# Performance work log

Hardware: AMD Instinct MI355X
Metric: run time of the kernel (lower is better)

Reference implementation:

```python
import jax, jax.numpy as jnp
import numpy as np

N_NODES = 100_000
N_EDGES = 1_600_000
D_IN = 128
D_HID = 64   # hard-coded hidden width in Embedder.__init__
D_OUT = 128  # embed_dim
N_GRAPHS = 512


def setup_inputs() -> dict:
    key = jax.random.key(0)
    ks = jax.random.split(key, 10)
    x = jax.random.normal(ks[0], (N_NODES, D_IN), dtype=jnp.float32)
    edge_index = jax.random.randint(ks[1], (2, N_EDGES), 0, N_NODES, dtype=jnp.int64)
    batch_index = jnp.sort(jax.random.randint(ks[2], (N_NODES,), 0, N_GRAPHS, dtype=jnp.int64))
    def glorot(k, fan_in, fan_out):
        s = 1.0 / np.sqrt(fan_in)
        return jax.random.uniform(k, (fan_in, fan_out), jnp.float32, -s, s)
    # layer 1: SAGEConv(D_IN -> D_HID); layer 2: SAGEConv(D_HID -> D_OUT)
    return {
        "x": x,
        "W1_l": glorot(ks[3], D_IN, D_HID),   # applied to mean-aggregated neighbors
        "W1_r": glorot(ks[4], D_IN, D_HID),   # applied to root node
        "b1": jnp.zeros((D_HID,), jnp.float32),
        "W2_l": glorot(ks[5], D_HID, D_OUT),
        "W2_r": glorot(ks[6], D_HID, D_OUT),
        "b2": jnp.zeros((D_OUT,), jnp.float32),
        "edge_index": edge_index,
        "batch_index": batch_index,
    }


def _sage_conv(x, edge_index, W_l, W_r, b):
    # PyG SAGEConv with mean aggregation:
    # out_i = (mean_{j in N(i)} x_j) @ W_l + x_i @ W_r + b
    src, dst = edge_index[0], edge_index[1]
    n = x.shape[0]
    agg = jax.ops.segment_sum(x[src], dst, num_segments=n)          # [N, F]
    deg = jax.ops.segment_sum(jnp.ones((src.shape[0],), x.dtype), dst, num_segments=n)
    mean_nbr = agg / jnp.maximum(deg, 1.0)[:, None]
    return mean_nbr @ W_l + x @ W_r + b


def reference(x, W1_l, W1_r, b1, W2_l, W2_r, b2, edge_index, batch_index):
    h = _sage_conv(x, edge_index, W1_l, W1_r, b1)
    h = jax.nn.relu(h)
    h = _sage_conv(h, edge_index, W2_l, W2_r, b2)
    # F.dropout(p=0.5, training=False) -> identity in eval mode
    # gap: global mean pool per graph
    sums = jax.ops.segment_sum(h, batch_index, num_segments=N_GRAPHS)
    cnts = jax.ops.segment_sum(jnp.ones((h.shape[0],), h.dtype), batch_index, num_segments=N_GRAPHS)
    return sums / jnp.maximum(cnts, 1.0)[:, None]
```

## Files before the change

kernel.cpp:

```cpp
#include <hip/hip_runtime.h>

#define NN   100000
#define NE   1600000
#define DIN  128
#define DH   64
#define DOUT 128
#define NG   512

#define NB   391
#define EPB  6250
#define MSZ  (NB*256)

typedef short short8 __attribute__((ext_vector_type(8)));
typedef float floatx4 __attribute__((ext_vector_type(4)));

__device__ __forceinline__ unsigned short f2bf(float f) {
  unsigned b = __float_as_uint(f);
  b += 0x7FFF + ((b >> 16) & 1);
  return (unsigned short)(b >> 16);
}
__device__ __forceinline__ float bflo(unsigned u) {
  return __uint_as_float(u << 16);
}
__device__ __forceinline__ float bfhi(unsigned u) {
  return __uint_as_float(u & 0xFFFF0000u);
}
__device__ __forceinline__ unsigned pack2(float a, float b) {
  return (unsigned)f2bf(a) | ((unsigned)f2bf(b) << 16);
}

__global__ __launch_bounds__(256) void prep_kernel(
    const int* __restrict__ dst, int* __restrict__ cnt,
    const float* __restrict__ W1l, const float* __restrict__ W1r,
    short* __restrict__ wfrag, const int* __restrict__ batch,
    int* __restrict__ gs) {
  __shared__ int h[NB];
  int b = blockIdx.x;
  if (b < 256) {
    for (int i = threadIdx.x; i < NB; i += 256) h[i] = 0;
    __syncthreads();
    int start = b * EPB, end = start + EPB;
    for (int e = start + threadIdx.x; e < end; e += 256)
      atomicAdd(&h[dst[e] >> 8], 1);
    __syncthreads();
    for (int bb = threadIdx.x; bb < NB; bb += 256)
      cnt[bb * 256 + b] = h[bb];
  } else if (b == 256) {
    for (int i = threadIdx.x; i < DIN * DH; i += 256) {
      int k = i >> 6, n = i & 63;
      int kt = k >> 5, kin = k & 31;
      int lane = ((kin >> 3) << 4) | (n & 15);
      int j8 = kin & 7;
      int jt = n >> 4;
      float wl = W1l[i], wr = W1r[i];
      unsigned bl_ = __float_as_uint(wl);
      unsigned br_ = __float_as_uint(wr);
      short hl = (short)(bl_ >> 16);
      short hr = (short)(br_ >> 16);
      float rl = wl - __uint_as_float(bl_ & 0xFFFF0000u);
      float rr = wr - __uint_as_float(br_ & 0xFFFF0000u);
      short ll = (short)(__float_as_uint(rl) >> 16);
      short lr = (short)(__float_as_uint(rr) >> 16);
      int base0 = (((kt * 2 + 0) * 4 + jt) * 2) * 512 + lane * 8 + j8;
      int base1 = (((kt * 2 + 1) * 4 + jt) * 2) * 512 + lane * 8 + j8;
      wfrag[base0]       = hl;
      wfrag[base0 + 512] = ll;
      wfrag[base1]       = hr;
      wfrag[base1 + 512] = lr;
    }
  } else {
    for (int g = threadIdx.x; g <= NG; g += 256) {
      if (g == NG) { gs[NG] = NN; continue; }
      int lo = 0, hi = NN;
      while (lo < hi) {
        int mid = (lo + hi) >> 1;
        if (batch[mid] < g) lo = mid + 1; else hi = mid;
      }
      gs[g] = lo;
    }
  }
}

__global__ __launch_bounds__(256) void reduce_kernel(
    const int* __restrict__ cnt, int* __restrict__ partials) {
  __shared__ int s[256];
  int i = blockIdx.x * 256 + threadIdx.x;
  s[threadIdx.x] = cnt[i];
  __syncthreads();
  for (int off = 128; off > 0; off >>= 1) {
    if (threadIdx.x < off) s[threadIdx.x] += s[threadIdx.x + off];
    __syncthreads();
  }
  if (threadIdx.x == 0) partials[blockIdx.x] = s[0];
}

__global__ __launch_bounds__(256) void scanpart_kernel(int* __restrict__ partials) {
  __shared__ int s[NB];
  for (int i = threadIdx.x; i < NB; i += 256) s[i] = partials[i];
  __syncthreads();
  if (threadIdx.x == 0) {
    int run = 0;
    for (int i = 0; i < NB; ++i) { int v = s[i]; s[i] = run; run += v; }
  }
  __syncthreads();
  for (int i = threadIdx.x; i < NB; i += 256) partials[i] = s[i];
}

__global__ __launch_bounds__(256) void scanfinal_kernel(
    const int* __restrict__ cnt, const int* __restrict__ partials,
    int* __restrict__ scanned) {
  __shared__ int s[256];
  int t = threadIdx.x;
  int i = blockIdx.x * 256 + t;
  int c = cnt[i];
  s[t] = c;
  __syncthreads();
  for (int off = 1; off < 256; off <<= 1) {
    int v = (t >= off) ? s[t - off] : 0;
    __syncthreads();
    s[t] += v;
    __syncthreads();
  }
  scanned[i] = s[t] - c + partials[blockIdx.x];
}

__global__ __launch_bounds__(256, 4) void proj_part_kernel(
    const int* __restrict__ src, const int* __restrict__ dst,
    const int* __restrict__ scanned, int* __restrict__ part,
    const float* __restrict__ x, const short* __restrict__ wfrag,
    const float* __restrict__ b1, unsigned short* __restrict__ xlb,
    unsigned short* __restrict__ xrb) {
  __shared__ short sB[16384];
  if (blockIdx.x < 256) {
    int* cur = (int*)sB;
    for (int i = threadIdx.x; i < NB; i += 256)
      cur[i] = scanned[i * 256 + blockIdx.x];
    __syncthreads();
    int start = blockIdx.x * EPB, end = start + EPB;
    for (int e = start + threadIdx.x; e < end; e += 256) {
      int d = dst[e], s = src[e];
      int pos = atomicAdd(&cur[d >> 8], 1);
      part[pos] = ((d & 255) << 17) | s;
    }
    return;
  }
  int wave = threadIdx.x >> 6;
  int lane = threadIdx.x & 63;
  int m = lane & 15, q = lane >> 4;
  int tpair = (blockIdx.x - 256) * 4 + wave;
  int tile0 = tpair * 2, tile1 = tile0 + 1;
  bool act0 = tile0 < 6250;
  bool act1 = tile1 < 6250;
  int t0c = act0 ? tile0 : 6249;
  int t1c = act1 ? tile1 : 6249;

  int r0 = t0c * 16 + m;
  int r1 = t1c * 16 + m;
  const float4* xa = (const float4*)x + (size_t)r0 * 32 + q * 2;
  const float4* xb = (const float4*)x + (size_t)r1 * 32 + q * 2;

  floatx4 acc0[8], acc1[8];
#pragma unroll
  for (int a = 0; a < 8; ++a) {
    acc0[a] = (floatx4){0.f, 0.f, 0.f, 0.f};
    acc1[a] = (floatx4){0.f, 0.f, 0.f, 0.f};
  }

  const float4* wf4 = (const float4*)wfrag;
  float4* sB4 = (float4*)sB;

#pragma unroll 1
  for (int stage = 0; stage < 2; ++stage) {
    if (stage) __syncthreads();
    for (int i = threadIdx.x; i < 2048; i += 256)
      sB4[i] = wf4[stage * 2048 + i];
    __syncthreads();

#pragma unroll
    for (int kk = 0; kk < 2; ++kk) {
      int kt = stage * 2 + kk;
      float4 p0 = xa[kt * 8];
      float4 p1 = xa[kt * 8 + 1];
      float4 p2 = xb[kt * 8];
      float4 p3 = xb[kt * 8 + 1];
      float af0[8] = {p0.x, p0.y, p0.z, p0.w, p1.x, p1.y, p1.z, p1.w};
      float af1[8] = {p2.x, p2.y, p2.z, p2.w, p3.x, p3.y, p3.z, p3.w};
      short8 ah0, al0, ah1, al1;
#pragma unroll
      for (int e = 0; e < 8; ++e) {
        unsigned b0 = __float_as_uint(af0[e]);
        ah0[e] = (short)(b0 >> 16);
        float lo0 = af0[e] - __uint_as_float(b0 & 0xFFFF0000u);
        al0[e] = (short)(__float_as_uint(lo0) >> 16);
        unsigned b1_ = __float_as_uint(af1[e]);
        ah1[e] = (short)(b1_ >> 16);
        float lo1 = af1[e] - __uint_as_float(b1_ & 0xFFFF0000u);
        al1[e] = (short)(__float_as_uint(lo1) >> 16);
      }
#pragma unroll
      for (int mat = 0; mat < 2; ++mat) {
#pragma unroll
        for (int jt = 0; jt < 4; ++jt) {
          int unit = ((kk * 2 + mat) * 4 + jt) * 2;
          short8 bh = *(const short8*)(sB + unit * 512 + lane * 8);
          short8 bl = *(const short8*)(sB + (unit + 1) * 512 + lane * 8);
          floatx4 c0 = acc0[mat * 4 + jt];
          c0 = __builtin_amdgcn_mfma_f32_16x16x32_bf16(ah0, bh, c0, 0, 0, 0);
          c0 = __builtin_amdgcn_mfma_f32_16x16x32_bf16(ah0, bl, c0, 0, 0, 0);
          c0 = __builtin_amdgcn_mfma_f32_16x16x32_bf16(al0, bh, c0, 0, 0, 0);
          acc0[mat * 4 + jt] = c0;
          floatx4 c1 = acc1[mat * 4 + jt];
          c1 = __builtin_amdgcn_mfma_f32_16x16x32_bf16(ah1, bh, c1, 0, 0, 0);
          c1 = __builtin_amdgcn_mfma_f32_16x16x32_bf16(ah1, bl, c1, 0, 0, 0);
          c1 = __builtin_amdgcn_mfma_f32_16x16x32_bf16(al1, bh, c1, 0, 0, 0);
          acc1[mat * 4 + jt] = c1;
        }
      }
    }
  }

#pragma unroll
  for (int jt = 0; jt < 4; ++jt) {
    int j = jt * 16 + m;
    float bj = b1[j];
    floatx4 cl0 = acc0[jt], cr0 = acc0[4 + jt];
    floatx4 cl1 = acc1[jt], cr1 = acc1[4 + jt];
    if (act0) {
#pragma unroll
      for (int r = 0; r < 4; ++r) {
        int n0 = tile0 * 16 + q * 4 + r;
        xlb[(size_t)n0 * DH + j] = f2bf(cl0[r]);
        xrb[(size_t)n0 * DH + j] = f2bf(cr0[r] + bj);
      }
    }
    if (act1) {
#pragma unroll
      for (int r = 0; r < 4; ++r) {
        int n1 = tile1 * 16 + q * 4 + r;
        xlb[(size_t)n1 * DH + j] = f2bf(cl1[r]);
        xrb[(size_t)n1 * DH + j] = f2bf(cr1[r] + bj);
      }
    }
  }
}

__global__ __launch_bounds__(256) void bucket_csr_kernel(
    const int* __restrict__ part, const int* __restrict__ scanned,
    int* __restrict__ row_start, int* __restrict__ eidx) {
  int b = blockIdx.x, t = threadIdx.x;
  int ebeg = scanned[b * 256];
  int eend = (b == NB - 1) ? NE : scanned[(b + 1) * 256];
  int nbase = b << 8;
  int nloc = NN - nbase; if (nloc > 256) nloc = 256;
  __shared__ int cntL[256];
  __shared__ int exclL[256];
  cntL[t] = 0;
  __syncthreads();
  for (int e = ebeg + t; e < eend; e += 256)
    atomicAdd(&cntL[part[e] >> 17], 1);
  __syncthreads();
  int c = cntL[t];
  exclL[t] = c;
  __syncthreads();
  for (int off = 1; off < 256; off <<= 1) {
    int v = (t >= off) ? exclL[t - off] : 0;
    __syncthreads();
    exclL[t] += v;
    __syncthreads();
  }
  int excl = exclL[t] - c;
  if (t < nloc) row_start[nbase + t] = ebeg + excl;
  if (b == NB - 1 && t == 0) row_start[NN] = NE;
  cntL[t] = excl;
  __syncthreads();
  for (int e = ebeg + t; e < eend; e += 256) {
    int v = part[e];
    int pos = atomicAdd(&cntL[v >> 17], 1);
    eidx[ebeg + pos] = v & 0x1FFFF;
  }
}

template <bool RELU_ADD>
__global__ __launch_bounds__(256) void gather_kernel(
    const uint4* __restrict__ feat4, const int* __restrict__ row_start,
    const int* __restrict__ eidx, const uint4* __restrict__ xr4,
    uint4* __restrict__ out4) {
  int t = blockIdx.x * 256 + threadIdx.x;
  int node = t >> 3;
  if (node >= NN) return;
  int fl = t & 7;
  int rs = row_start[node], re = row_start[node + 1];
  float a0 = 0.f, a1 = 0.f, a2 = 0.f, a3 = 0.f;
  float a4 = 0.f, a5 = 0.f, a6 = 0.f, a7 = 0.f;
  int k = rs;
  for (; k + 8 <= re; k += 8) {
    uint4 v[8];
#pragma unroll
    for (int u = 0; u < 8; ++u) v[u] = feat4[(size_t)eidx[k + u] * 8 + fl];
#pragma unroll
    for (int u = 0; u < 8; ++u) {
      a0 += bflo(v[u].x); a1 += bfhi(v[u].x);
      a2 += bflo(v[u].y); a3 += bfhi(v[u].y);
      a4 += bflo(v[u].z); a5 += bfhi(v[u].z);
      a6 += bflo(v[u].w); a7 += bfhi(v[u].w);
    }
  }
  for (; k + 2 <= re; k += 2) {
    uint4 v0 = feat4[(size_t)eidx[k] * 8 + fl];
    uint4 v1 = feat4[(size_t)eidx[k + 1] * 8 + fl];
    a0 += bflo(v0.x) + bflo(v1.x); a1 += bfhi(v0.x) + bfhi(v1.x);
    a2 += bflo(v0.y) + bflo(v1.y); a3 += bfhi(v0.y) + bfhi(v1.y);
    a4 += bflo(v0.z) + bflo(v1.z); a5 += bfhi(v0.z) + bfhi(v1.z);
    a6 += bflo(v0.w) + bflo(v1.w); a7 += bfhi(v0.w) + bfhi(v1.w);
  }
  if (k < re) {
    uint4 v = feat4[(size_t)eidx[k] * 8 + fl];
    a0 += bflo(v.x); a1 += bfhi(v.x);
    a2 += bflo(v.y); a3 += bfhi(v.y);
    a4 += bflo(v.z); a5 += bfhi(v.z);
    a6 += bflo(v.w); a7 += bfhi(v.w);
  }
  float inv = 1.0f / fmaxf((float)(re - rs), 1.0f);
  a0 *= inv; a1 *= inv; a2 *= inv; a3 *= inv;
  a4 *= inv; a5 *= inv; a6 *= inv; a7 *= inv;
  if (RELU_ADD) {
    uint4 r = xr4[(size_t)node * 8 + fl];
    a0 = fmaxf(a0 + bflo(r.x), 0.f); a1 = fmaxf(a1 + bfhi(r.x), 0.f);
    a2 = fmaxf(a2 + bflo(r.y), 0.f); a3 = fmaxf(a3 + bfhi(r.y), 0.f);
    a4 = fmaxf(a4 + bflo(r.z), 0.f); a5 = fmaxf(a5 + bfhi(r.z), 0.f);
    a6 = fmaxf(a6 + bflo(r.w), 0.f); a7 = fmaxf(a7 + bfhi(r.w), 0.f);
  }
  uint4 o;
  o.x = pack2(a0, a1);
  o.y = pack2(a2, a3);
  o.z = pack2(a4, a5);
  o.w = pack2(a6, a7);
  out4[(size_t)node * 8 + fl] = o;
}

__global__ __launch_bounds__(256) void pool_final_kernel(
    const unsigned* __restrict__ hb2, const unsigned* __restrict__ mb2,
    const int* __restrict__ gs, const float* __restrict__ W2l,
    const float* __restrict__ W2r, const float* __restrict__ b2,
    float* __restrict__ out) {
  int g = blockIdx.x;
  int start = gs[g], end = gs[g + 1];
  int slot = threadIdx.x >> 5;
  int j2   = threadIdx.x & 31;
  float sh0 = 0.f, sh1 = 0.f, sm0 = 0.f, sm1 = 0.f;
  for (int n = start + slot; n < end; n += 8) {
    unsigned hv = hb2[(size_t)n * 32 + j2];
    unsigned mv = mb2[(size_t)n * 32 + j2];
    sh0 += bflo(hv); sh1 += bfhi(hv);
    sm0 += bflo(mv); sm1 += bfhi(mv);
  }
  __shared__ float redh[8][DH];
  __shared__ float redm[8][DH];
  redh[slot][j2 * 2] = sh0; redh[slot][j2 * 2 + 1] = sh1;
  redm[slot][j2 * 2] = sm0; redm[slot][j2 * 2 + 1] = sm1;
  __syncthreads();
  __shared__ float hsL[DH], msL[DH];
  if (threadIdx.x < DH) {
    float a = 0.f, b = 0.f;
#pragma unroll
    for (int s = 0; s < 8; ++s) { a += redh[s][threadIdx.x]; b += redm[s][threadIdx.x]; }
    hsL[threadIdx.x] = a; msL[threadIdx.x] = b;
  }
  __syncthreads();
  int j = threadIdx.x;
  if (j < DOUT) {
    float n = (float)(end - start);
    float acc = 0.f;
#pragma unroll 8
    for (int k = 0; k < DH; ++k)
      acc += msL[k] * W2l[k * DOUT + j] + hsL[k] * W2r[k * DOUT + j];
    out[g * DOUT + j] = (acc + n * b2[j]) / fmaxf(n, 1.0f);
  }
}

extern "C" void kernel_launch(void* const* d_in, const int* in_sizes, int n_in,
                              void* d_out, int out_size, void* d_ws, size_t ws_size,
                              hipStream_t stream) {
  (void)in_sizes; (void)n_in; (void)out_size; (void)ws_size;
  const float* x   = (const float*)d_in[0];
  const float* W1l = (const float*)d_in[1];
  const float* W1r = (const float*)d_in[2];
  const float* b1  = (const float*)d_in[3];
  const float* W2l = (const float*)d_in[4];
  const float* W2r = (const float*)d_in[5];
  const float* b2  = (const float*)d_in[6];
  const int*   ei  = (const int*)d_in[7];
  const int*   batch = (const int*)d_in[8];
  const int* src = ei;
  const int* dst = ei + NE;
  float* out = (float*)d_out;

  char* ws = (char*)d_ws;
  unsigned short* xlb = (unsigned short*)(ws);
  unsigned short* hb  = (unsigned short*)(ws + 12800000);
  unsigned short* mb  = (unsigned short*)(ws + 25600000);
  unsigned short* xrb = (unsigned short*)(ws + 38400000);
  int*  part      = (int*)(ws + 51200000);
  int*  cnt       = (int*)(ws + 57600000);
  int*  scanned   = (int*)(ws + 58000384);
  int*  eidx      = (int*)(ws + 76800000);
  int*  row_start = (int*)(ws + 83200000);
  int*   gs       = (int*)(ws + 83600128);
  short* wfrag    = (short*)(ws + 83900032);
  int*  partials  = (int*)(ws + 84400128);

  const int gBlocks = (NN * 8 + 255) / 256;

  prep_kernel<<<258, 256, 0, stream>>>(dst, cnt, W1l, W1r, wfrag, batch, gs);
  reduce_kernel<<<NB, 256, 0, stream>>>(cnt, partials);
  scanpart_kernel<<<1, 256, 0, stream>>>(partials);
  scanfinal_kernel<<<NB, 256, 0, stream>>>(cnt, partials, scanned);

  proj_part_kernel<<<1038, 256, 0, stream>>>(src, dst, scanned, part,
                                             x, wfrag, b1, xlb, xrb);
  bucket_csr_kernel<<<NB, 256, 0, stream>>>(part, scanned, row_start, eidx);

  gather_kernel<true><<<gBlocks, 256, 0, stream>>>(
      (const uint4*)xlb, row_start, eidx, (const uint4*)xrb, (uint4*)hb);

  gather_kernel<false><<<gBlocks, 256, 0, stream>>>(
      (const uint4*)hb, row_start, eidx, nullptr, (uint4*)mb);

  pool_final_kernel<<<NG, 256, 0, stream>>>(
      (const unsigned*)hb, (const unsigned*)mb, gs, W2l, W2r, b2, out);
}
```

Measured before the change: 244.7 us.

## Split fused projection/partition kernel into separate proj and part kernels

Separates the edge-partition work from the MFMA projection that were co-scheduled in one heterogeneous launch. The projection now handles one 16-row tile per wave instead of two, which lowers register pressure and allows a higher occupancy hint. Partitioning runs as its own launch with 1024-thread blocks. This gives up the overlap of the memory-bound partition with the compute-bound projection and adds one launch, in exchange for simpler, better-occupied kernels.

```diff
diff --git a/kernel.cpp b/kernel.cpp
--- a/kernel.cpp
+++ b/kernel.cpp
@@ -124,47 +124,40 @@
   scanned[i] = s[t] - c + partials[blockIdx.x];
 }
 
-__global__ __launch_bounds__(256, 4) void proj_part_kernel(
+__global__ __launch_bounds__(1024) void part_kernel(
     const int* __restrict__ src, const int* __restrict__ dst,
-    const int* __restrict__ scanned, int* __restrict__ part,
+    const int* __restrict__ scanned, int* __restrict__ part) {
+  __shared__ int cur[NB];
+  int b = blockIdx.x;
+  for (int i = threadIdx.x; i < NB; i += 1024)
+    cur[i] = scanned[i * 256 + b];
+  __syncthreads();
+  int start = b * EPB, end = start + EPB;
+  for (int e = start + threadIdx.x; e < end; e += 1024) {
+    int d = dst[e], s = src[e];
+    int pos = atomicAdd(&cur[d >> 8], 1);
+    part[pos] = ((d & 255) << 17) | s;
+  }
+}
+
+__global__ __launch_bounds__(256, 5) void proj_kernel(
     const float* __restrict__ x, const short* __restrict__ wfrag,
     const float* __restrict__ b1, unsigned short* __restrict__ xlb,
     unsigned short* __restrict__ xrb) {
   __shared__ short sB[16384];
-  if (blockIdx.x < 256) {
-    int* cur = (int*)sB;
-    for (int i = threadIdx.x; i < NB; i += 256)
-      cur[i] = scanned[i * 256 + blockIdx.x];
-    __syncthreads();
-    int start = blockIdx.x * EPB, end = start + EPB;
-    for (int e = start + threadIdx.x; e < end; e += 256) {
-      int d = dst[e], s = src[e];
-      int pos = atomicAdd(&cur[d >> 8], 1);
-      part[pos] = ((d & 255) << 17) | s;
-    }
-    return;
-  }
   int wave = threadIdx.x >> 6;
   int lane = threadIdx.x & 63;
   int m = lane & 15, q = lane >> 4;
-  int tpair = (blockIdx.x - 256) * 4 + wave;
-  int tile0 = tpair * 2, tile1 = tile0 + 1;
-  bool act0 = tile0 < 6250;
-  bool act1 = tile1 < 6250;
-  int t0c = act0 ? tile0 : 6249;
-  int t1c = act1 ? tile1 : 6249;
-
-  int r0 = t0c * 16 + m;
-  int r1 = t1c * 16 + m;
+  int tile = blockIdx.x * 4 + wave;
+  bool act = tile < 6250;
+  int tc = act ? tile : 6249;
+
+  int r0 = tc * 16 + m;
   const float4* xa = (const float4*)x + (size_t)r0 * 32 + q * 2;
-  const float4* xb = (const float4*)x + (size_t)r1 * 32 + q * 2;
-
-  floatx4 acc0[8], acc1[8];
-#pragma unroll
-  for (int a = 0; a < 8; ++a) {
-    acc0[a] = (floatx4){0.f, 0.f, 0.f, 0.f};
-    acc1[a] = (floatx4){0.f, 0.f, 0.f, 0.f};
-  }
+
+  floatx4 acc[8];
+#pragma unroll
+  for (int a = 0; a < 8; ++a) acc[a] = (floatx4){0.f, 0.f, 0.f, 0.f};
 
   const float4* wf4 = (const float4*)wfrag;
   float4* sB4 = (float4*)sB;
@@ -181,21 +174,14 @@
       int kt = stage * 2 + kk;
       float4 p0 = xa[kt * 8];
       float4 p1 = xa[kt * 8 + 1];
-      float4 p2 = xb[kt * 8];
-      float4 p3 = xb[kt * 8 + 1];
       float af0[8] = {p0.x, p0.y, p0.z, p0.w, p1.x, p1.y, p1.z, p1.w};
-      float af1[8] = {p2.x, p2.y, p2.z, p2.w, p3.x, p3.y, p3.z, p3.w};
-      short8 ah0, al0, ah1, al1;
+      short8 ah, al;
 #pragma unroll
       for (int e = 0; e < 8; ++e) {
         unsigned b0 = __float_as_uint(af0[e]);
-        ah0[e] = (short)(b0 >> 16);
+        ah[e] = (short)(b0 >> 16);
         float lo0 = af0[e] - __uint_as_float(b0 & 0xFFFF0000u);
-        al0[e] = (short)(__float_as_uint(lo0) >> 16);
-        unsigned b1_ = __float_as_uint(af1[e]);
-        ah1[e] = (short)(b1_ >> 16);
-        float lo1 = af1[e] - __uint_as_float(b1_ & 0xFFFF0000u);
-        al1[e] = (short)(__float_as_uint(lo1) >> 16);
+        al[e] = (short)(__float_as_uint(lo0) >> 16);
       }
 #pragma unroll
       for (int mat = 0; mat < 2; ++mat) {
@@ -204,41 +190,27 @@
           int unit = ((kk * 2 + mat) * 4 + jt) * 2;
           short8 bh = *(const short8*)(sB + unit * 512 + lane * 8);
           short8 bl = *(const short8*)(sB + (unit + 1) * 512 + lane * 8);
-          floatx4 c0 = acc0[mat * 4 + jt];
-          c0 = __builtin_amdgcn_mfma_f32_16x16x32_bf16(ah0, bh, c0, 0, 0, 0);
-          c0 = __builtin_amdgcn_mfma_f32_16x16x32_bf16(ah0, bl, c0, 0, 0, 0);
-          c0 = __builtin_amdgcn_mfma_f32_16x16x32_bf16(al0, bh, c0, 0, 0, 0);
-          acc0[mat * 4 + jt] = c0;
-          floatx4 c1 = acc1[mat * 4 + jt];
-          c1 = __builtin_amdgcn_mfma_f32_16x16x32_bf16(ah1, bh, c1, 0, 0, 0);
-          c1 = __builtin_amdgcn_mfma_f32_16x16x32_bf16(ah1, bl, c1, 0, 0, 0);
-          c1 = __builtin_amdgcn_mfma_f32_16x16x32_bf16(al1, bh, c1, 0, 0, 0);
-          acc1[mat * 4 + jt] = c1;
+          floatx4 c = acc[mat * 4 + jt];
+          c = __builtin_amdgcn_mfma_f32_16x16x32_bf16(ah, bh, c, 0, 0, 0);
+          c = __builtin_amdgcn_mfma_f32_16x16x32_bf16(ah, bl, c, 0, 0, 0);
+          c = __builtin_amdgcn_mfma_f32_16x16x32_bf16(al, bh, c, 0, 0, 0);
+          acc[mat * 4 + jt] = c;
         }
       }
     }
   }
 
-#pragma unroll
-  for (int jt = 0; jt < 4; ++jt) {
-    int j = jt * 16 + m;
-    float bj = b1[j];
-    floatx4 cl0 = acc0[jt], cr0 = acc0[4 + jt];
-    floatx4 cl1 = acc1[jt], cr1 = acc1[4 + jt];
-    if (act0) {
+  if (act) {
+#pragma unroll
+    for (int jt = 0; jt < 4; ++jt) {
+      int j = jt * 16 + m;
+      float bj = b1[j];
+      floatx4 cl = acc[jt], cr = acc[4 + jt];
 #pragma unroll
       for (int r = 0; r < 4; ++r) {
-        int n0 = tile0 * 16 + q * 4 + r;
-        xlb[(size_t)n0 * DH + j] = f2bf(cl0[r]);
-        xrb[(size_t)n0 * DH + j] = f2bf(cr0[r] + bj);
-      }
-    }
-    if (act1) {
-#pragma unroll
-      for (int r = 0; r < 4; ++r) {
-        int n1 = tile1 * 16 + q * 4 + r;
-        xlb[(size_t)n1 * DH + j] = f2bf(cl1[r]);
-        xrb[(size_t)n1 * DH + j] = f2bf(cr1[r] + bj);
+        int n0 = tile * 16 + q * 4 + r;
+        xlb[(size_t)n0 * DH + j] = f2bf(cl[r]);
+        xrb[(size_t)n0 * DH + j] = f2bf(cr[r] + bj);
       }
     }
   }
@@ -416,8 +388,8 @@
   scanpart_kernel<<<1, 256, 0, stream>>>(partials);
   scanfinal_kernel<<<NB, 256, 0, stream>>>(cnt, partials, scanned);
 
-  proj_part_kernel<<<1038, 256, 0, stream>>>(src, dst, scanned, part,
-                                             x, wfrag, b1, xlb, xrb);
+  proj_kernel<<<1563, 256, 0, stream>>>(x, wfrag, b1, xlb, xrb);
+  part_kernel<<<256, 1024, 0, stream>>>(src, dst, scanned, part);
   bucket_csr_kernel<<<NB, 256, 0, stream>>>(part, scanned, row_start, eidx);
 
   gather_kernel<true><<<gBlocks, 256, 0, stream>>>(
```

Measured after the change: 252.1 us. 1.03x slower.

## Fuse second-layer neighbor gather into per-graph pooling kernel

Applied to the files above, without the earlier changes.

The second mean-aggregation gather is folded into the pooling kernel. Each graph's block now computes neighbor means on the fly and accumulates them directly into the pooled sums, so the intermediate aggregated feature buffer is never written to or read back from memory, and one launch is removed. Parallelism drops from about 3000 blocks to 512 blocks of 1024 threads. Graphs of uneven size could leave work imbalanced across those blocks.

```diff
diff --git a/kernel.cpp b/kernel.cpp
--- a/kernel.cpp
+++ b/kernel.cpp
@@ -338,43 +338,91 @@
   out4[(size_t)node * 8 + fl] = o;
 }
 
-__global__ __launch_bounds__(256) void pool_final_kernel(
-    const unsigned* __restrict__ hb2, const unsigned* __restrict__ mb2,
+__global__ __launch_bounds__(1024) void gather2_pool_kernel(
+    const uint4* __restrict__ feat4,
+    const int* __restrict__ row_start, const int* __restrict__ eidx,
     const int* __restrict__ gs, const float* __restrict__ W2l,
     const float* __restrict__ W2r, const float* __restrict__ b2,
     float* __restrict__ out) {
   int g = blockIdx.x;
   int start = gs[g], end = gs[g + 1];
-  int slot = threadIdx.x >> 5;
-  int j2   = threadIdx.x & 31;
-  float sh0 = 0.f, sh1 = 0.f, sm0 = 0.f, sm1 = 0.f;
-  for (int n = start + slot; n < end; n += 8) {
-    unsigned hv = hb2[(size_t)n * 32 + j2];
-    unsigned mv = mb2[(size_t)n * 32 + j2];
-    sh0 += bflo(hv); sh1 += bfhi(hv);
-    sm0 += bflo(mv); sm1 += bfhi(mv);
-  }
-  __shared__ float redh[8][DH];
-  __shared__ float redm[8][DH];
-  redh[slot][j2 * 2] = sh0; redh[slot][j2 * 2 + 1] = sh1;
-  redm[slot][j2 * 2] = sm0; redm[slot][j2 * 2 + 1] = sm1;
-  __syncthreads();
-  __shared__ float hsL[DH], msL[DH];
+  int slot = threadIdx.x >> 3;
+  int fl   = threadIdx.x & 7;
+  float sm[8], sh[8];
+#pragma unroll
+  for (int i = 0; i < 8; ++i) { sm[i] = 0.f; sh[i] = 0.f; }
+
+  for (int n = start + slot; n < end; n += 128) {
+    int rs = row_start[n], re = row_start[n + 1];
+    float a0 = 0.f, a1 = 0.f, a2 = 0.f, a3 = 0.f;
+    float a4 = 0.f, a5 = 0.f, a6 = 0.f, a7 = 0.f;
+    int k = rs;
+    for (; k + 4 <= re; k += 4) {
+      uint4 v[4];
+#pragma unroll
+      for (int u = 0; u < 4; ++u) v[u] = feat4[(size_t)eidx[k + u] * 8 + fl];
+#pragma unroll
+      for (int u = 0; u < 4; ++u) {
+        a0 += bflo(v[u].x); a1 += bfhi(v[u].x);
+        a2 += bflo(v[u].y); a3 += bfhi(v[u].y);
+        a4 += bflo(v[u].z); a5 += bfhi(v[u].z);
+        a6 += bflo(v[u].w); a7 += bfhi(v[u].w);
+      }
+    }
+    for (; k < re; ++k) {
+      uint4 v = feat4[(size_t)eidx[k] * 8 + fl];
+      a0 += bflo(v.x); a1 += bfhi(v.x);
+      a2 += bflo(v.y); a3 += bfhi(v.y);
+      a4 += bflo(v.z); a5 += bfhi(v.z);
+      a6 += bflo(v.w); a7 += bfhi(v.w);
+    }
+    float inv = 1.0f / fmaxf((float)(re - rs), 1.0f);
+    sm[0] += a0 * inv; sm[1] += a1 * inv; sm[2] += a2 * inv; sm[3] += a3 * inv;
+    sm[4] += a4 * inv; sm[5] += a5 * inv; sm[6] += a6 * inv; sm[7] += a7 * inv;
+    uint4 hv = feat4[(size_t)n * 8 + fl];
+    sh[0] += bflo(hv.x); sh[1] += bfhi(hv.x);
+    sh[2] += bflo(hv.y); sh[3] += bfhi(hv.y);
+    sh[4] += bflo(hv.z); sh[5] += bfhi(hv.z);
+    sh[6] += bflo(hv.w); sh[7] += bfhi(hv.w);
+  }
+
+#pragma unroll
+  for (int off = 8; off <= 32; off <<= 1) {
+#pragma unroll
+    for (int i = 0; i < 8; ++i) {
+      sm[i] += __shfl_xor(sm[i], off);
+      sh[i] += __shfl_xor(sh[i], off);
+    }
+  }
+
+  __shared__ float redm[16][DH];
+  __shared__ float redh[16][DH];
+  int wv = threadIdx.x >> 6;
+  int lane = threadIdx.x & 63;
+  if (lane < 8) {
+#pragma unroll
+    for (int i = 0; i < 8; ++i) {
+      redm[wv][lane * 8 + i] = sm[i];
+      redh[wv][lane * 8 + i] = sh[i];
+    }
+  }
+  __syncthreads();
+  __shared__ float msL[DH], hsL[DH];
   if (threadIdx.x < DH) {
     float a = 0.f, b = 0.f;
 #pragma unroll
-    for (int s = 0; s < 8; ++s) { a += redh[s][threadIdx.x]; b += redm[s][threadIdx.x]; }
-    hsL[threadIdx.x] = a; msL[threadIdx.x] = b;
+    for (int w = 0; w < 16; ++w) { a += redm[w][threadIdx.x]; b += redh[w][threadIdx.x]; }
+    msL[threadIdx.x] = a; hsL[threadIdx.x] = b;
   }
   __syncthreads();
   int j = threadIdx.x;
   if (j < DOUT) {
-    float n = (float)(end - start);
+    float n_ = (float)(end - start);
     float acc = 0.f;
 #pragma unroll 8
     for (int k = 0; k < DH; ++k)
       acc += msL[k] * W2l[k * DOUT + j] + hsL[k] * W2r[k * DOUT + j];
-    out[g * DOUT + j] = (acc + n * b2[j]) / fmaxf(n, 1.0f);
+    out[g * DOUT + j] = (acc + n_ * b2[j]) / fmaxf(n_, 1.0f);
   }
 }
 
@@ -398,7 +446,6 @@
   char* ws = (char*)d_ws;
   unsigned short* xlb = (unsigned short*)(ws);
   unsigned short* hb  = (unsigned short*)(ws + 12800000);
-  unsigned short* mb  = (unsigned short*)(ws + 25600000);
   unsigned short* xrb = (unsigned short*)(ws + 38400000);
   int*  part      = (int*)(ws + 51200000);
   int*  cnt       = (int*)(ws + 57600000);
@@ -423,9 +470,6 @@
   gather_kernel<true><<<gBlocks, 256, 0, stream>>>(
       (const uint4*)xlb, row_start, eidx, (const uint4*)xrb, (uint4*)hb);
 
-  gather_kernel<false><<<gBlocks, 256, 0, stream>>>(
-      (const uint4*)hb, row_start, eidx, nullptr, (uint4*)mb);
-
-  pool_final_kernel<<<NG, 256, 0, stream>>>(
-      (const unsigned*)hb, (const unsigned*)mb, gs, W2l, W2r, b2, out);
-}
+  gather2_pool_kernel<<<NG, 1024, 0, stream>>>(
+      (const uint4*)hb, row_start, eidx, gs, W2l, W2r, b2, out);
+}
```

Measured after the change: 242.3 us. Within noise of the previous version (-1.0%).
